# Kernel optimization log

Hardware: AMD Instinct MI355X
Metric: run time of the kernel (lower is better)

## Reference

```python
import jax, jax.numpy as jnp
import numpy as np

D_MODEL = 1024
NUM_HEADS = 16
D_K = D_MODEL // NUM_HEADS
THETA = 10000.0
NEG_INF = -1e9


def _rope(x, positions):
    # x: [B, H, S, d_k]; rotate interleaved (even, odd) pairs as complex mult
    half = D_K // 2
    inv_freq = 1.0 / (THETA ** (jnp.arange(0, D_K, 2, dtype=jnp.float32) / D_K))  # [half]
    angles = positions.astype(jnp.float32)[:, None] * inv_freq  # [S, half]
    cos, sin = jnp.cos(angles), jnp.sin(angles)
    xe = x[..., 0::2]
    xo = x[..., 1::2]
    re = xe * cos - xo * sin
    ro = xe * sin + xo * cos
    return jnp.stack([re, ro], axis=-1).reshape(x.shape).astype(x.dtype)


def setup_inputs() -> dict:
    key = jax.random.key(0)
    ks = jax.random.split(key, 5)
    sigma = np.sqrt(2.0 / (D_MODEL + D_MODEL))
    x = jax.random.normal(ks[0], (2, 2048, D_MODEL), dtype=jnp.float32)
    mk = lambda k: (sigma * jax.random.normal(k, (D_MODEL, D_MODEL))).astype(jnp.float32)
    return {
        "x": x,
        "Wq": mk(ks[1]), "bq": jnp.zeros((D_MODEL,), jnp.float32),
        "Wk": mk(ks[2]), "bk": jnp.zeros((D_MODEL,), jnp.float32),
        "Wv": mk(ks[3]), "bv": jnp.zeros((D_MODEL,), jnp.float32),
        "Wo": mk(ks[4]), "bo": jnp.zeros((D_MODEL,), jnp.float32),
        "token_positions": jnp.arange(2048, dtype=jnp.int64) if jax.config.jax_enable_x64 else jnp.arange(2048, dtype=jnp.int32),
    }


def reference(x, Wq, bq, Wk, bk, Wv, bv, Wo, bo, token_positions):
    B, S, D = x.shape
    # Linear stores weight as [in, out] and computes x @ W.T + b
    Q = x @ Wq.T + bq
    K = x @ Wk.T + bk
    V = x @ Wv.T + bv
    def split_heads(t):  # [B,S,D] -> [B,H,S,d_k]
        return t.reshape(B, S, NUM_HEADS, D_K).transpose(0, 2, 1, 3)
    Q, K, V = split_heads(Q), split_heads(K), split_heads(V)
    # the torch forward always uses arange positions (it overwrites token_positions)
    pos = jnp.arange(S)
    Q = _rope(Q, pos)
    K = _rope(K, pos)
    scale = 1.0 / jnp.sqrt(jnp.float32(D_K))
    scores = jnp.einsum("bhqd,bhkd->bhqk", Q, K) * scale
    causal = jnp.tril(jnp.ones((S, S), dtype=bool))  # allowed where key <= query
    scores = jnp.where(causal, scores, NEG_INF)
    weights = jax.nn.softmax(scores, axis=-1)
    attn = jnp.einsum("bhqk,bhkd->bhqd", weights, V)  # [B,H,S,d_k]
    concat = attn.transpose(0, 2, 1, 3).reshape(B, S, D)
    return concat @ Wo.T + bo
```

## Files before the change

kernel.cpp:

```cpp
#include <hip/hip_runtime.h>
#include <hip/hip_bf16.h>
#include <math.h>

#define D_MODEL 1024
#define NH      16
#define DK      64
#define SEQ     2048
#define BATCH   2
#define RTOT    (BATCH*SEQ)

typedef __attribute__((ext_vector_type(8))) short bf16x8;
typedef __attribute__((ext_vector_type(4))) float f32x4;

__device__ __forceinline__ float bf2f(unsigned short u) {
    union { unsigned int i; float f; } v; v.i = ((unsigned int)u) << 16; return v.f;
}
__device__ __forceinline__ unsigned short f2bf(float f) {
    union { float f; unsigned int i; } v; v.f = f;
    unsigned int r = v.i + 0x7FFFu + ((v.i >> 16) & 1u);
    return (unsigned short)(r >> 16);
}
__device__ __forceinline__ unsigned short f2bf_hw(float f) {
    __hip_bfloat16 h = __float2bfloat16(f);
    union { __hip_bfloat16 h; unsigned short u; } v; v.h = h; return v.u;
}
__device__ __forceinline__ unsigned int pack2bf(float a, float b) {
    return (unsigned int)f2bf(a) | ((unsigned int)f2bf(b) << 16);
}

__device__ __forceinline__ void gload_lds16(const unsigned short* g,
                                            unsigned short* l) {
    __builtin_amdgcn_global_load_lds(
        (const __attribute__((address_space(1))) void*)g,
        (__attribute__((address_space(3))) void*)l, 16, 0, 0);
}

__device__ __forceinline__ void stage128x32(
    const unsigned short* __restrict__ src, int ldk,
    unsigned short* lds, int w, int lane)
{
    #pragma unroll
    for (int p = 0; p < 2; ++p) {
        const int ckb = (w * 2 + p) * 64;
        const int ck  = ckb + lane;
        const int row = ck >> 2;
        const int cs  = (ck & 3) ^ ((row >> 1) & 3);
        gload_lds16(src + (size_t)row * ldk + cs * 8, lds + (size_t)ckb * 8);
    }
}

__global__ __launch_bounds__(256) void prep(
    const float* __restrict__ X,  const float* __restrict__ Wq,
    const float* __restrict__ Wk, const float* __restrict__ Wv,
    const float* __restrict__ Wo,
    unsigned short* __restrict__ Xbf, unsigned short* __restrict__ Wqkvbf,
    unsigned short* __restrict__ Wobf, float2* __restrict__ rope)
{
    const int id = blockIdx.x * 256 + threadIdx.x;
    const float* src;
    unsigned short* dst;
    size_t off;
    if (id < 524288) {
        src = X; dst = Xbf; off = (size_t)id * 8;
    } else {
        const int j   = id - 524288;
        const int mat = j >> 17;
        off = (size_t)(j & 131071) * 8;
        src = (mat == 0) ? Wq : (mat == 1) ? Wk : (mat == 2) ? Wv : Wo;
        dst = (mat < 3) ? (Wqkvbf + (size_t)mat * 1048576) : Wobf;
    }
    const float4 a = *(const float4*)&src[off];
    const float4 b = *(const float4*)&src[off + 4];
    uint4 p;
    p.x = pack2bf(a.x, a.y); p.y = pack2bf(a.z, a.w);
    p.z = pack2bf(b.x, b.y); p.w = pack2bf(b.z, b.w);
    *(uint4*)&dst[off] = p;

    if (id < SEQ * 32) {
        const int s  = id >> 5;
        const int fi = id & 31;
        const float ang = (float)s * powf(10000.0f, -(float)(2 * fi) * (1.0f / 64.0f));
        float c, sn;
        sincosf(ang, &c, &sn);
        rope[id] = make_float2(c, sn);
    }
}

__global__ __launch_bounds__(256) void gemm_qkv_bf(
    const unsigned short* __restrict__ Xb, const unsigned short* __restrict__ Wall,
    const float* __restrict__ bq, const float* __restrict__ bk,
    const float* __restrict__ bv, const float2* __restrict__ rope,
    unsigned short* __restrict__ Qw, unsigned short* __restrict__ Kw,
    unsigned short* __restrict__ Vw)
{
    __shared__ unsigned short Ab[2][128 * 32];
    __shared__ unsigned short Bb[2][128 * 32];

    const int t   = threadIdx.x;
    const int lin = blockIdx.y * 24 + blockIdx.x;
    const int swz = (lin & 7) * 96 + (lin >> 3);
    const int ct  = swz % 24;
    const int mat  = ct >> 3;
    const int col0 = (ct & 7) * 128;
    const int row0 = (swz / 24) * 128;

    const unsigned short* W = Wall + (size_t)mat * 1048576;
    const float* bias = (mat == 0) ? bq : (mat == 1) ? bk : bv;
    unsigned short* Y = (mat == 0) ? Qw : (mat == 1) ? Kw : Vw;

    const int lane = t & 63;
    const int wave = t >> 6;
    const int wm   = (wave >> 1) * 64;
    const int wn   = (wave & 1) * 64;
    const int l15  = lane & 15;
    const int quad = lane >> 4;

    f32x4 acc[4][4];
    #pragma unroll
    for (int i = 0; i < 4; ++i)
        #pragma unroll
        for (int j = 0; j < 4; ++j) acc[i][j] = (f32x4){0.f, 0.f, 0.f, 0.f};

    const unsigned short* Asrc = &Xb[(size_t)row0 * D_MODEL];
    const unsigned short* Bsrc = &W[(size_t)col0 * D_MODEL];

    stage128x32(Asrc, D_MODEL, Ab[0], wave, lane);
    stage128x32(Bsrc, D_MODEL, Bb[0], wave, lane);
    __syncthreads();

    for (int kt = 0; kt < 32; ++kt) {
        const int cur = kt & 1;
        if (kt + 1 < 32) {
            stage128x32(Asrc + (kt + 1) * 32, D_MODEL, Ab[cur ^ 1], wave, lane);
            stage128x32(Bsrc + (kt + 1) * 32, D_MODEL, Bb[cur ^ 1], wave, lane);
        }
        bf16x8 af[4], bfr[4];
        #pragma unroll
        for (int i = 0; i < 4; ++i) {
            const int r = wm + i * 16 + l15;
            af[i] = *(const bf16x8*)&Ab[cur][r * 32 + ((quad ^ ((r >> 1) & 3)) * 8)];
        }
        #pragma unroll
        for (int j = 0; j < 4; ++j) {
            const int r = wn + j * 16 + l15;
            bfr[j] = *(const bf16x8*)&Bb[cur][r * 32 + ((quad ^ ((r >> 1) & 3)) * 8)];
        }
        #pragma unroll
        for (int i = 0; i < 4; ++i)
            #pragma unroll
            for (int j = 0; j < 4; ++j)
                acc[i][j] = __builtin_amdgcn_mfma_f32_16x16x32_bf16(
                    af[i], bfr[j], acc[i][j], 0, 0, 0);
        __syncthreads();
    }

    #pragma unroll
    for (int i = 0; i < 4; ++i) {
        #pragma unroll
        for (int j = 0; j < 4; ++j) {
            const int cl = col0 + wn + j * 16 + l15;
            const int h  = cl >> 6;
            const int dk = cl & 63;
            const int fi = (cl & 63) >> 1;
            const float bsv = bias[cl];
            #pragma unroll
            for (int r = 0; r < 4; ++r) {
                const int row = row0 + wm + i * 16 + quad * 4 + r;
                const int s   = row & (SEQ - 1);
                const int b   = row >> 11;
                float v = acc[i][j][r] + bsv;
                if (mat == 0) v *= 0.125f;
                if (mat < 2) {
                    const float2 cs = rope[s * 32 + fi];
                    const float p = __shfl_xor(v, 1, 64);
                    v = v * cs.x + ((l15 & 1) ? -p * cs.y : p * cs.y);
                }
                Y[((size_t)(b * NH + h) * SEQ + s) * DK + dk] = f2bf(v);
            }
        }
    }
}

__global__ __launch_bounds__(256) void gemm_qkv_f32(
    const float* __restrict__ X,
    const float* __restrict__ Wq, const float* __restrict__ bq,
    const float* __restrict__ Wk, const float* __restrict__ bk,
    const float* __restrict__ Wv, const float* __restrict__ bv,
    unsigned short* __restrict__ Qw, unsigned short* __restrict__ Kw,
    unsigned short* __restrict__ Vw)
{
    __shared__ unsigned short Ab[128 * 40];
    __shared__ unsigned short Bb[128 * 40];

    const int t    = threadIdx.x;
    const int ct   = blockIdx.x;
    const int mat  = ct >> 3;
    const int col0 = (ct & 7) * 128;
    const int row0 = blockIdx.y * 128;

    const float* W    = (mat == 0) ? Wq : (mat == 1) ? Wk : Wv;
    const float* bias = (mat == 0) ? bq : (mat == 1) ? bk : bv;
    unsigned short* Y = (mat == 0) ? Qw : (mat == 1) ? Kw : Vw;

    const int srow  = t >> 1;
    const int skseg = (t & 1) * 16;

    const int lane = t & 63;
    const int wave = t >> 6;
    const int wm   = (wave >> 1) * 64;
    const int wn   = (wave & 1) * 64;
    const int l15  = lane & 15;
    const int quad = lane >> 4;

    f32x4 acc[4][4];
    #pragma unroll
    for (int i = 0; i < 4; ++i)
        #pragma unroll
        for (int j = 0; j < 4; ++j) acc[i][j] = (f32x4){0.f, 0.f, 0.f, 0.f};

    for (int k0 = 0; k0 < D_MODEL; k0 += 32) {
        const float* xs = &X[(size_t)(row0 + srow) * D_MODEL + k0 + skseg];
        const float* ws = &W[(size_t)(col0 + srow) * D_MODEL + k0 + skseg];
        float4 x0 = *(const float4*)&xs[0],  x1 = *(const float4*)&xs[4];
        float4 x2 = *(const float4*)&xs[8],  x3 = *(const float4*)&xs[12];
        float4 w0 = *(const float4*)&ws[0],  w1 = *(const float4*)&ws[4];
        float4 w2 = *(const float4*)&ws[8],  w3 = *(const float4*)&ws[12];
        uint4 pa0, pa1, pb0, pb1;
        pa0.x = pack2bf(x0.x, x0.y); pa0.y = pack2bf(x0.z, x0.w);
        pa0.z = pack2bf(x1.x, x1.y); pa0.w = pack2bf(x1.z, x1.w);
        pa1.x = pack2bf(x2.x, x2.y); pa1.y = pack2bf(x2.z, x2.w);
        pa1.z = pack2bf(x3.x, x3.y); pa1.w = pack2bf(x3.z, x3.w);
        pb0.x = pack2bf(w0.x, w0.y); pb0.y = pack2bf(w0.z, w0.w);
        pb0.z = pack2bf(w1.x, w1.y); pb0.w = pack2bf(w1.z, w1.w);
        pb1.x = pack2bf(w2.x, w2.y); pb1.y = pack2bf(w2.z, w2.w);
        pb1.z = pack2bf(w3.x, w3.y); pb1.w = pack2bf(w3.z, w3.w);
        __syncthreads();
        *(uint4*)&Ab[srow * 40 + skseg]     = pa0;
        *(uint4*)&Ab[srow * 40 + skseg + 8] = pa1;
        *(uint4*)&Bb[srow * 40 + skseg]     = pb0;
        *(uint4*)&Bb[srow * 40 + skseg + 8] = pb1;
        __syncthreads();

        bf16x8 af[4], bfr[4];
        #pragma unroll
        for (int i = 0; i < 4; ++i)
            af[i] = *(const bf16x8*)&Ab[(wm + i * 16 + l15) * 40 + quad * 8];
        #pragma unroll
        for (int j = 0; j < 4; ++j)
            bfr[j] = *(const bf16x8*)&Bb[(wn + j * 16 + l15) * 40 + quad * 8];
        #pragma unroll
        for (int i = 0; i < 4; ++i)
            #pragma unroll
            for (int j = 0; j < 4; ++j)
                acc[i][j] = __builtin_amdgcn_mfma_f32_16x16x32_bf16(
                    af[i], bfr[j], acc[i][j], 0, 0, 0);
    }

    float invj[4];
    #pragma unroll
    for (int j = 0; j < 4; ++j) {
        const int cl = col0 + wn + j * 16 + l15;
        const int fi = (cl & 63) >> 1;
        invj[j] = powf(10000.0f, -(float)(2 * fi) * (1.0f / 64.0f));
    }
    #pragma unroll
    for (int i = 0; i < 4; ++i) {
        #pragma unroll
        for (int j = 0; j < 4; ++j) {
            const int cl = col0 + wn + j * 16 + l15;
            const int h  = cl >> 6;
            const int dk = cl & 63;
            const float bsv = bias[cl];
            #pragma unroll
            for (int r = 0; r < 4; ++r) {
                const int row = row0 + wm + i * 16 + quad * 4 + r;
                const int s   = row & (SEQ - 1);
                const int b   = row >> 11;
                float v = acc[i][j][r] + bsv;
                if (mat == 0) v *= 0.125f;
                if (mat < 2) {
                    float c, sn;
                    sincosf((float)s * invj[j], &c, &sn);
                    const float p = __shfl_xor(v, 1, 64);
                    v = v * c + ((l15 & 1) ? -p * sn : p * sn);
                }
                Y[((size_t)(b * NH + h) * SEQ + s) * DK + dk] = f2bf(v);
            }
        }
    }
}

__global__ __launch_bounds__(256) void gemm_out_bf(
    const unsigned short* __restrict__ A, const unsigned short* __restrict__ W,
    const float* __restrict__ bias, float* __restrict__ out)
{
    __shared__ unsigned short Ab[2][128 * 32];
    __shared__ unsigned short Bb[2][128 * 32];

    const int t   = threadIdx.x;
    const int lin = blockIdx.y * 8 + blockIdx.x;
    const int swz = (lin & 7) * 32 + (lin >> 3);
    const int col0 = (swz & 7) * 128;
    const int row0 = (swz >> 3) * 128;

    const int lane = t & 63;
    const int wave = t >> 6;
    const int wm   = (wave >> 1) * 64;
    const int wn   = (wave & 1) * 64;
    const int l15  = lane & 15;
    const int quad = lane >> 4;

    f32x4 acc[4][4];
    #pragma unroll
    for (int i = 0; i < 4; ++i)
        #pragma unroll
        for (int j = 0; j < 4; ++j) acc[i][j] = (f32x4){0.f, 0.f, 0.f, 0.f};

    const unsigned short* Asrc = &A[(size_t)row0 * D_MODEL];
    const unsigned short* Bsrc = &W[(size_t)col0 * D_MODEL];

    stage128x32(Asrc, D_MODEL, Ab[0], wave, lane);
    stage128x32(Bsrc, D_MODEL, Bb[0], wave, lane);
    __syncthreads();

    for (int kt = 0; kt < 32; ++kt) {
        const int cur = kt & 1;
        if (kt + 1 < 32) {
            stage128x32(Asrc + (kt + 1) * 32, D_MODEL, Ab[cur ^ 1], wave, lane);
            stage128x32(Bsrc + (kt + 1) * 32, D_MODEL, Bb[cur ^ 1], wave, lane);
        }
        bf16x8 af[4], bfr[4];
        #pragma unroll
        for (int i = 0; i < 4; ++i) {
            const int r = wm + i * 16 + l15;
            af[i] = *(const bf16x8*)&Ab[cur][r * 32 + ((quad ^ ((r >> 1) & 3)) * 8)];
        }
        #pragma unroll
        for (int j = 0; j < 4; ++j) {
            const int r = wn + j * 16 + l15;
            bfr[j] = *(const bf16x8*)&Bb[cur][r * 32 + ((quad ^ ((r >> 1) & 3)) * 8)];
        }
        #pragma unroll
        for (int i = 0; i < 4; ++i)
            #pragma unroll
            for (int j = 0; j < 4; ++j)
                acc[i][j] = __builtin_amdgcn_mfma_f32_16x16x32_bf16(
                    af[i], bfr[j], acc[i][j], 0, 0, 0);
        __syncthreads();
    }

    #pragma unroll
    for (int i = 0; i < 4; ++i) {
        #pragma unroll
        for (int j = 0; j < 4; ++j) {
            const int col = col0 + wn + j * 16 + l15;
            const float bsv = bias[col];
            #pragma unroll
            for (int r = 0; r < 4; ++r) {
                const int row = row0 + wm + i * 16 + quad * 4 + r;
                out[(size_t)row * D_MODEL + col] = acc[i][j][r] + bsv;
            }
        }
    }
}

__global__ __launch_bounds__(256) void gemm_out_f32(
    const unsigned short* __restrict__ A, const float* __restrict__ W,
    const float* __restrict__ bias, float* __restrict__ out)
{
    __shared__ unsigned short Ab[128 * 40];
    __shared__ unsigned short Bb[128 * 40];

    const int t    = threadIdx.x;
    const int col0 = blockIdx.x * 128;
    const int row0 = blockIdx.y * 128;

    const int srow  = t >> 1;
    const int skseg = (t & 1) * 16;

    const int lane = t & 63;
    const int wave = t >> 6;
    const int wm   = (wave >> 1) * 64;
    const int wn   = (wave & 1) * 64;
    const int l15  = lane & 15;
    const int quad = lane >> 4;

    f32x4 acc[4][4];
    #pragma unroll
    for (int i = 0; i < 4; ++i)
        #pragma unroll
        for (int j = 0; j < 4; ++j) acc[i][j] = (f32x4){0.f, 0.f, 0.f, 0.f};

    for (int k0 = 0; k0 < D_MODEL; k0 += 32) {
        const unsigned short* as = &A[(size_t)(row0 + srow) * D_MODEL + k0 + skseg];
        uint4 ua0 = *(const uint4*)&as[0];
        uint4 ua1 = *(const uint4*)&as[8];
        const float* ws = &W[(size_t)(col0 + srow) * D_MODEL + k0 + skseg];
        float4 w0 = *(const float4*)&ws[0],  w1 = *(const float4*)&ws[4];
        float4 w2 = *(const float4*)&ws[8],  w3 = *(const float4*)&ws[12];
        uint4 pb0, pb1;
        pb0.x = pack2bf(w0.x, w0.y); pb0.y = pack2bf(w0.z, w0.w);
        pb0.z = pack2bf(w1.x, w1.y); pb0.w = pack2bf(w1.z, w1.w);
        pb1.x = pack2bf(w2.x, w2.y); pb1.y = pack2bf(w2.z, w2.w);
        pb1.z = pack2bf(w3.x, w3.y); pb1.w = pack2bf(w3.z, w3.w);
        __syncthreads();
        *(uint4*)&Ab[srow * 40 + skseg]     = ua0;
        *(uint4*)&Ab[srow * 40 + skseg + 8] = ua1;
        *(uint4*)&Bb[srow * 40 + skseg]     = pb0;
        *(uint4*)&Bb[srow * 40 + skseg + 8] = pb1;
        __syncthreads();

        bf16x8 af[4], bfr[4];
        #pragma unroll
        for (int i = 0; i < 4; ++i)
            af[i] = *(const bf16x8*)&Ab[(wm + i * 16 + l15) * 40 + quad * 8];
        #pragma unroll
        for (int j = 0; j < 4; ++j)
            bfr[j] = *(const bf16x8*)&Bb[(wn + j * 16 + l15) * 40 + quad * 8];
        #pragma unroll
        for (int i = 0; i < 4; ++i)
            #pragma unroll
            for (int j = 0; j < 4; ++j)
                acc[i][j] = __builtin_amdgcn_mfma_f32_16x16x32_bf16(
                    af[i], bfr[j], acc[i][j], 0, 0, 0);
    }

    #pragma unroll
    for (int i = 0; i < 4; ++i) {
        #pragma unroll
        for (int j = 0; j < 4; ++j) {
            const int col = col0 + wn + j * 16 + l15;
            const float bsv = bias[col];
            #pragma unroll
            for (int r = 0; r < 4; ++r) {
                const int row = row0 + wm + i * 16 + quad * 4 + r;
                out[(size_t)row * D_MODEL + col] = acc[i][j][r] + bsv;
            }
        }
    }
}

#define DEFER_THR 16.0f

__device__ __forceinline__ void attn_tile_proc(
    const f32x4* sc, const bf16x8* vf,
    float& m, f32x4& lsum, f32x4* od,
    bool diag, int wq, int l15, int quad)
{
    float s[4][4];
    float pmax = -3.0e38f;
    #pragma unroll
    for (int kc = 0; kc < 4; ++kc) {
        const int kbase = 8 * quad + 4 * (kc & 1) + 32 * (kc >> 1);
        #pragma unroll
        for (int r = 0; r < 4; ++r) {
            float v = sc[kc][r];
            if (diag && (kbase + r > wq * 16 + l15)) v = -1.0e9f;
            s[kc][r] = v;
            pmax = fmaxf(pmax, v);
        }
    }
    pmax = fmaxf(pmax, __shfl_xor(pmax, 16, 64));
    pmax = fmaxf(pmax, __shfl_xor(pmax, 32, 64));

    if (!__all(pmax <= m + DEFER_THR)) {
        const float mnew  = fmaxf(m, pmax);
        const float alpha = __expf(m - mnew);
        m = mnew;
        #pragma unroll
        for (int r = 0; r < 4; ++r) {
            const float ar = __shfl(alpha, quad * 20 + r, 64);
            lsum[r] *= ar;
            #pragma unroll
            for (int dt = 0; dt < 4; ++dt) od[dt][r] *= ar;
        }
    }

    bf16x8 pa0, pa1;
    #pragma unroll
    for (int kc = 0; kc < 4; ++kc) {
        #pragma unroll
        for (int r = 0; r < 4; ++r) {
            const unsigned short b = f2bf_hw(__expf(s[kc][r] - m));
            const int e = 4 * (kc & 1) + r;
            if ((kc >> 1) == 0) pa0[e] = (short)b;
            else                pa1[e] = (short)b;
        }
    }

    bf16x8 ones;
    #pragma unroll
    for (int e = 0; e < 8; ++e) ones[e] = (short)0x3F80;

    __builtin_amdgcn_s_setprio(1);
    f32x4 rs = (f32x4){0.f, 0.f, 0.f, 0.f};
    rs = __builtin_amdgcn_mfma_f32_16x16x32_bf16(pa0, ones, rs, 0, 0, 0);
    rs = __builtin_amdgcn_mfma_f32_16x16x32_bf16(pa1, ones, rs, 0, 0, 0);
    #pragma unroll
    for (int dt = 0; dt < 4; ++dt) {
        od[dt] = __builtin_amdgcn_mfma_f32_16x16x32_bf16(pa0, vf[dt * 2],     od[dt], 0, 0, 0);
        od[dt] = __builtin_amdgcn_mfma_f32_16x16x32_bf16(pa1, vf[dt * 2 + 1], od[dt], 0, 0, 0);
    }
    __builtin_amdgcn_s_setprio(0);

    #pragma unroll
    for (int r = 0; r < 4; ++r) lsum[r] += rs[r];
}

__global__ __launch_bounds__(512) void attn_kernel(
    const unsigned short* __restrict__ Q, const unsigned short* __restrict__ K,
    const unsigned short* __restrict__ V, unsigned short* __restrict__ Out)
{
    __shared__ unsigned short Ks[2][64 * 72];
    __shared__ unsigned short Vt[2][64 * 72];

    const int lin = blockIdx.y * 16 + blockIdx.x;
    const int swz = (lin & 7) * 64 + (lin >> 3);
    const int qtA = swz & 15;
    const int qtB = (SEQ / 64 - 1) - qtA;
    const int bh  = swz >> 4;
    const unsigned short* Qb = Q + (size_t)bh * SEQ * DK;
    const unsigned short* Kb = K + (size_t)bh * SEQ * DK;
    const unsigned short* Vb = V + (size_t)bh * SEQ * DK;

    const int t    = threadIdx.x;
    const int lane = t & 63;
    const int w    = t >> 6;
    const int wq   = w & 3;
    const int qt   = (w < 4) ? qtA : qtB;
    const int l15  = lane & 15;
    const int quad = lane >> 4;

    const int qrow = qt * 64 + wq * 16 + l15;
    bf16x8 q0 = *(const bf16x8*)&Qb[(size_t)qrow * DK + quad * 8];
    bf16x8 q1 = *(const bf16x8*)&Qb[(size_t)qrow * DK + 32 + quad * 8];

    f32x4 od[4];
    f32x4 ls = (f32x4){0.f, 0.f, 0.f, 0.f};
    float m = -3.0e38f;
    #pragma unroll
    for (int r = 0; r < 4; ++r) od[r] = (f32x4){0.f, 0.f, 0.f, 0.f};

    const int tk = t >> 3;
    const int tc = t & 7;

    const int kp0 = tk ^ (tc * 8);
    const int ksw = (tk >> 3) & 3;
    const int kc0 = ((tc & 4) | ((tc & 3) ^ ksw)) * 8;

    bf16x8 kv0 = *(const bf16x8*)&Kb[((size_t)tk) * DK + tc * 8];
    bf16x8 vv0 = *(const bf16x8*)&Vb[((size_t)tk) * DK + tc * 8];

    *(bf16x8*)&Ks[0][tk * 72 + kc0] = kv0;
    #pragma unroll
    for (int e = 0; e < 8; ++e)
        Vt[0][(tc * 8 + e) * 72 + kp0] = (unsigned short)vv0[e];
    kv0 = *(const bf16x8*)&Kb[((size_t)(64 + tk)) * DK + tc * 8];
    vv0 = *(const bf16x8*)&Vb[((size_t)(64 + tk)) * DK + tc * 8];
    __syncthreads();

    for (int j = 0; j <= qtB; ++j) {
        const int cur = j & 1;

        if (j < qtB) {
            *(bf16x8*)&Ks[cur ^ 1][tk * 72 + kc0] = kv0;
            #pragma unroll
            for (int e = 0; e < 8; ++e)
                Vt[cur ^ 1][(tc * 8 + e) * 72 + kp0] = (unsigned short)vv0[e];
        }
        if (j + 2 <= qtB) {
            const size_t nb = (size_t)((j + 2) * 64);
            kv0 = *(const bf16x8*)&Kb[(nb + tk) * DK + tc * 8];
            vv0 = *(const bf16x8*)&Vb[(nb + tk) * DK + tc * 8];
        }

        if (j <= qt) {
            bf16x8 kf[8];
            #pragma unroll
            for (int kc = 0; kc < 4; ++kc) {
                const int kr = ((l15 >> 2) << 3) + ((kc & 1) << 2)
                             + ((kc >> 1) << 5) + (l15 & 3);
                const int cs = (quad ^ ((kr >> 3) & 3)) * 8;
                kf[kc * 2]     = *(const bf16x8*)&Ks[cur][kr * 72 + cs];
                kf[kc * 2 + 1] = *(const bf16x8*)&Ks[cur][kr * 72 + 32 + cs];
            }

            f32x4 sc[4];
            __builtin_amdgcn_s_setprio(1);
            #pragma unroll
            for (int kc = 0; kc < 4; ++kc) {
                f32x4 z = (f32x4){0.f, 0.f, 0.f, 0.f};
                z = __builtin_amdgcn_mfma_f32_16x16x32_bf16(kf[kc * 2],     q0, z, 0, 0, 0);
                z = __builtin_amdgcn_mfma_f32_16x16x32_bf16(kf[kc * 2 + 1], q1, z, 0, 0, 0);
                sc[kc] = z;
            }
            __builtin_amdgcn_s_setprio(0);

            bf16x8 vf[8];
            #pragma unroll
            for (int dt = 0; dt < 4; ++dt) {
                const int d  = dt * 16 + l15;
                const int sw = d & 0x38;
                vf[dt * 2]     = *(const bf16x8*)&Vt[cur][d * 72 + ((quad * 8) ^ sw)];
                vf[dt * 2 + 1] = *(const bf16x8*)&Vt[cur][d * 72 + ((32 + quad * 8) ^ sw)];
            }

            attn_tile_proc(sc, vf, m, ls, od, (j == qt), wq, l15, quad);
        }

        __syncthreads();
    }

    const int b = bh >> 4;
    const int h = bh & 15;
    #pragma unroll
    for (int r = 0; r < 4; ++r) {
        const float rl = 1.0f / ls[r];
        const int q = qt * 64 + wq * 16 + quad * 4 + r;
        #pragma unroll
        for (int dt = 0; dt < 4; ++dt)
            Out[((size_t)(b * SEQ + q)) * D_MODEL + h * DK + dt * 16 + l15] =
                f2bf(od[dt][r] * rl);
    }
}

extern "C" void kernel_launch(void* const* d_in, const int* in_sizes, int n_in,
                              void* d_out, int out_size, void* d_ws, size_t ws_size,
                              hipStream_t stream) {
    const float* x  = (const float*)d_in[0];
    const float* Wq = (const float*)d_in[1];
    const float* bq = (const float*)d_in[2];
    const float* Wk = (const float*)d_in[3];
    const float* bk = (const float*)d_in[4];
    const float* Wv = (const float*)d_in[5];
    const float* bv = (const float*)d_in[6];
    const float* Wo = (const float*)d_in[7];
    const float* bo = (const float*)d_in[8];

    const size_t E = (size_t)RTOT * D_MODEL;
    float* out = (float*)d_out;
    dim3 blk(256);

    const size_t WS_NEED = (4 * E + 4 * (size_t)D_MODEL * D_MODEL) * 2
                         + (size_t)SEQ * 32 * sizeof(float2);

    unsigned short* Qws = (unsigned short*)d_ws;
    unsigned short* Kws = Qws + E;
    unsigned short* Vws = Kws + E;
    unsigned short* AXs = Vws + E;

    if (ws_size >= WS_NEED) {
        unsigned short* Wqkv = AXs + E;
        unsigned short* Wobf = Wqkv + (size_t)3 * D_MODEL * D_MODEL;
        float2*         rope = (float2*)(Wobf + (size_t)D_MODEL * D_MODEL);

        prep<<<4096, blk, 0, stream>>>(x, Wq, Wk, Wv, Wo, AXs, Wqkv, Wobf, rope);

        dim3 gq(24, RTOT / 128);
        gemm_qkv_bf<<<gq, blk, 0, stream>>>(AXs, Wqkv, bq, bk, bv, rope,
                                            Qws, Kws, Vws);

        dim3 ga(SEQ / 128, BATCH * NH);
        attn_kernel<<<ga, dim3(512), 0, stream>>>(Qws, Kws, Vws, AXs);

        dim3 go(D_MODEL / 128, RTOT / 128);
        gemm_out_bf<<<go, blk, 0, stream>>>(AXs, Wobf, bo, out);
    } else {
        dim3 gq(24, RTOT / 128);
        gemm_qkv_f32<<<gq, blk, 0, stream>>>(x, Wq, bq, Wk, bk, Wv, bv,
                                             Qws, Kws, Vws);

        dim3 ga(SEQ / 128, BATCH * NH);
        attn_kernel<<<ga, dim3(512), 0, stream>>>(Qws, Kws, Vws, AXs);

        dim3 go(D_MODEL / 128, RTOT / 128);
        gemm_out_f32<<<go, blk, 0, stream>>>(AXs, Wo, bo, out);
    }
}
```

Before: 208.4 us.

## Triple-buffer GEMM K-tiles with partial vmcnt waits instead of full barriers

The QKV and output projection GEMMs move from double to triple buffering of the A and B LDS tiles, prefetching two K-steps ahead. The full __syncthreads is replaced by explicit s_waitcnt vmcnt(4) plus s_barrier, so loads for the next-next tile can stay in flight across the barrier. This raises LDS use per block (48KB) and relies on stage128x32 issuing exactly 2 global loads per call per thread; if that count is wrong the hand-written waitcnt could race.

```diff
diff --git a/kernel.cpp b/kernel.cpp
--- a/kernel.cpp
+++ b/kernel.cpp
@@ -93,8 +93,8 @@
     unsigned short* __restrict__ Qw, unsigned short* __restrict__ Kw,
     unsigned short* __restrict__ Vw)
 {
-    __shared__ unsigned short Ab[2][128 * 32];
-    __shared__ unsigned short Bb[2][128 * 32];
+    __shared__ unsigned short Ab[3][128 * 32];
+    __shared__ unsigned short Bb[3][128 * 32];
 
     const int t   = threadIdx.x;
     const int lin = blockIdx.y * 24 + blockIdx.x;
@@ -124,15 +124,19 @@
     const unsigned short* Asrc = &Xb[(size_t)row0 * D_MODEL];
     const unsigned short* Bsrc = &W[(size_t)col0 * D_MODEL];
 
-    stage128x32(Asrc, D_MODEL, Ab[0], wave, lane);
-    stage128x32(Bsrc, D_MODEL, Bb[0], wave, lane);
-    __syncthreads();
+    stage128x32(Asrc,      D_MODEL, Ab[0], wave, lane);
+    stage128x32(Bsrc,      D_MODEL, Bb[0], wave, lane);
+    stage128x32(Asrc + 32, D_MODEL, Ab[1], wave, lane);
+    stage128x32(Bsrc + 32, D_MODEL, Bb[1], wave, lane);
+    asm volatile("s_waitcnt vmcnt(4)" ::: "memory");
+    __builtin_amdgcn_s_barrier();
 
     for (int kt = 0; kt < 32; ++kt) {
-        const int cur = kt & 1;
-        if (kt + 1 < 32) {
-            stage128x32(Asrc + (kt + 1) * 32, D_MODEL, Ab[cur ^ 1], wave, lane);
-            stage128x32(Bsrc + (kt + 1) * 32, D_MODEL, Bb[cur ^ 1], wave, lane);
+        const int cur = kt % 3;
+        if (kt + 2 < 32) {
+            const int nxt = (kt + 2) % 3;
+            stage128x32(Asrc + (kt + 2) * 32, D_MODEL, Ab[nxt], wave, lane);
+            stage128x32(Bsrc + (kt + 2) * 32, D_MODEL, Bb[nxt], wave, lane);
         }
         bf16x8 af[4], bfr[4];
         #pragma unroll
@@ -151,7 +155,9 @@
             for (int j = 0; j < 4; ++j)
                 acc[i][j] = __builtin_amdgcn_mfma_f32_16x16x32_bf16(
                     af[i], bfr[j], acc[i][j], 0, 0, 0);
-        __syncthreads();
+        if (kt + 2 < 32) asm volatile("s_waitcnt vmcnt(4) lgkmcnt(0)" ::: "memory");
+        else             asm volatile("s_waitcnt vmcnt(0) lgkmcnt(0)" ::: "memory");
+        __builtin_amdgcn_s_barrier();
     }
 
     #pragma unroll
@@ -294,8 +300,8 @@
     const unsigned short* __restrict__ A, const unsigned short* __restrict__ W,
     const float* __restrict__ bias, float* __restrict__ out)
 {
-    __shared__ unsigned short Ab[2][128 * 32];
-    __shared__ unsigned short Bb[2][128 * 32];
+    __shared__ unsigned short Ab[3][128 * 32];
+    __shared__ unsigned short Bb[3][128 * 32];
 
     const int t   = threadIdx.x;
     const int lin = blockIdx.y * 8 + blockIdx.x;
@@ -319,15 +325,19 @@
     const unsigned short* Asrc = &A[(size_t)row0 * D_MODEL];
     const unsigned short* Bsrc = &W[(size_t)col0 * D_MODEL];
 
-    stage128x32(Asrc, D_MODEL, Ab[0], wave, lane);
-    stage128x32(Bsrc, D_MODEL, Bb[0], wave, lane);
-    __syncthreads();
+    stage128x32(Asrc,      D_MODEL, Ab[0], wave, lane);
+    stage128x32(Bsrc,      D_MODEL, Bb[0], wave, lane);
+    stage128x32(Asrc + 32, D_MODEL, Ab[1], wave, lane);
+    stage128x32(Bsrc + 32, D_MODEL, Bb[1], wave, lane);
+    asm volatile("s_waitcnt vmcnt(4)" ::: "memory");
+    __builtin_amdgcn_s_barrier();
 
     for (int kt = 0; kt < 32; ++kt) {
-        const int cur = kt & 1;
-        if (kt + 1 < 32) {
-            stage128x32(Asrc + (kt + 1) * 32, D_MODEL, Ab[cur ^ 1], wave, lane);
-            stage128x32(Bsrc + (kt + 1) * 32, D_MODEL, Bb[cur ^ 1], wave, lane);
+        const int cur = kt % 3;
+        if (kt + 2 < 32) {
+            const int nxt = (kt + 2) % 3;
+            stage128x32(Asrc + (kt + 2) * 32, D_MODEL, Ab[nxt], wave, lane);
+            stage128x32(Bsrc + (kt + 2) * 32, D_MODEL, Bb[nxt], wave, lane);
         }
         bf16x8 af[4], bfr[4];
         #pragma unroll
@@ -346,7 +356,9 @@
             for (int j = 0; j < 4; ++j)
                 acc[i][j] = __builtin_amdgcn_mfma_f32_16x16x32_bf16(
                     af[i], bfr[j], acc[i][j], 0, 0, 0);
-        __syncthreads();
+        if (kt + 2 < 32) asm volatile("s_waitcnt vmcnt(4) lgkmcnt(0)" ::: "memory");
+        else             asm volatile("s_waitcnt vmcnt(0) lgkmcnt(0)" ::: "memory");
+        __builtin_amdgcn_s_barrier();
     }
 
     #pragma unroll
```

New measurement: 203.4 us. 2.4% less time.
